# Performance work log

Measured on AMD Instinct MI355X. Metric: run time of the kernel, lower is better.

## Reference

```python
import jax, jax.numpy as jnp
import numpy as np

NT = 32          # nt_states
T = 64           # t_states
ST = NT + T      # total states
NEG = -1e9       # matches self.huge fill


def setup_inputs() -> dict:
    key = jax.random.key(0)
    k1, k2, k3 = jax.random.split(key, 3)
    B, n = 8, 28
    return {
        "unary_scores": jax.random.normal(k1, (B, n, T), dtype=jnp.float32),
        "rule_scores": jax.random.normal(k2, (B, NT, ST, ST), dtype=jnp.float32),
        "root_scores": jax.random.normal(k3, (B, NT), dtype=jnp.float32),
    }


def _inside(unary_scores, rule_scores, root_scores):
    # Chart indexed beta[b, width, start, state]; span (s, s+w) lives at [b, w, s].
    # Invalid (state-range) slots hold NEG, so exp() underflows them to exactly 0,
    # reproducing the terminal/nonterminal slice logic of the torch code.
    B, n, _ = unary_scores.shape
    beta = jnp.full((B, n, n, ST), NEG, dtype=unary_scores.dtype)
    beta = beta.at[:, 0, :, NT:].set(unary_scores)  # width-0 diagonal: preterminals

    mrule = rule_scores.max(axis=(2, 3))                    # [B, A]
    erule = jnp.exp(rule_scores - mrule[:, :, None, None])  # [B, A, L, R]

    for w in range(1, n):
        S = n - w                     # number of valid start positions
        k = np.arange(w)              # split offset: u = s + k
        # left child: span (s, s+k) -> width k, start s
        left = beta[:, :w, :S, :]                                  # [B, w, S, ST]
        # right child: span (s+k+1, s+w) -> width w-1-k, start s+k+1
        sr = k[:, None] + 1 + np.arange(S)[None, :]                # [w, S]
        right = beta[:, (w - 1 - k)[:, None], sr, :]               # [B, w, S, ST]

        # stable logsumexp over (k, l, r) via exp-space matmuls
        ml = left.max(-1)                                          # [B, w, S]
        mr = right.max(-1)                                         # [B, w, S]
        M = (ml + mr).max(1)                                       # [B, S]
        el = jnp.exp(left - ml[..., None])
        er = jnp.exp(right - mr[..., None] + (ml + mr - M[:, None, :])[..., None])
        numer = jnp.einsum('bksl,bksr->bslr', el, er)              # [B, S, L, R]
        total = jnp.einsum('bslr,balr->bsa', numer, erule)         # [B, S, A]
        score = jnp.log(total) + M[..., None] + mrule[:, None, :]
        beta = beta.at[:, w, :S, :NT].set(score)

    top = beta[:, n - 1, 0, :NT] + root_scores                     # span (0, n-1)
    return jax.nn.logsumexp(top, axis=1)                           # log Z, [B]


def reference(unary_scores, rule_scores, root_scores):
    return _inside(unary_scores, rule_scores, root_scores)
```

## Files before the change

### kernel.cpp

```cpp
#include <hip/hip_runtime.h>
#include <cstdint>
#include <cstddef>


#define NMAX 28
#define SLOTT 864
#define SLOTN 3456

#define R_ELT 0
#define R_F   1856
#define R_G   5568
#define R_F2  9280
#define R_G2  12992
#define R_TRI 16704
#define R_BMX 22736
#define R_ENA 23520
#define C_TRI 0
#define C_BMX 6032
#define C_GPP 6816
#define C_ELK 7584
#define C_ERK 8608
#define C_NUM 14752
#define C_RED 16536
#define LDSF  27616

__device__ __forceinline__ int off32(int w, int n) {
    return (w - 1) * n - (w * (w - 1)) / 2;
}
__device__ __forceinline__ float gload(const float* p) {
    return __hip_atomic_load(p, __ATOMIC_RELAXED, __HIP_MEMORY_SCOPE_AGENT);
}
__device__ __forceinline__ void gstore(float* p, float v) {
    __hip_atomic_store(p, v, __ATOMIC_RELAXED, __HIP_MEMORY_SCOPE_AGENT);
}
__device__ __forceinline__ unsigned gloadu(const unsigned* p) {
    return __hip_atomic_load(p, __ATOMIC_RELAXED, __HIP_MEMORY_SCOPE_AGENT);
}
__device__ __forceinline__ void gstoreu(unsigned* p, unsigned v) {
    __hip_atomic_store(p, v, __ATOMIC_RELAXED, __HIP_MEMORY_SCOPE_AGENT);
}
__device__ __forceinline__ float dot4acc(float4 m, float4 t, float acc) {
    return fmaf(m.x, t.x, fmaf(m.y, t.y, fmaf(m.z, t.z, fmaf(m.w, t.w, acc))));
}
__device__ __forceinline__ float b2f(unsigned short u) {
    return __uint_as_float(((unsigned)u) << 16);
}
__device__ __forceinline__ unsigned short f2b(float x) {
    unsigned u = __float_as_uint(x);
    return (unsigned short)((u + 0x7fffu + ((u >> 16) & 1u)) >> 16);
}
__device__ __forceinline__ float maxM(const float* bmx, int w, int s) {
    float M = -3.0e38f;
    for (int k = 0; k < w; ++k)
        M = fmaxf(M, bmx[k * NMAX + s] + bmx[(w - 1 - k) * NMAX + s + k + 1]);
    return M;
}
__device__ __forceinline__ float maxMc(const float* bmx, int w, int s) {
    float M = -3.0e38f;
    for (int k = 2; k <= w - 3; ++k)
        M = fmaxf(M, bmx[k * NMAX + s] + bmx[(w - 1 - k) * NMAX + s + k + 1]);
    return M;
}
__device__ __forceinline__ void finalize_row(float* lds, int triOff, int bmxOff,
                                             const float* slot, int wf, int n,
                                             int tid) {
    int Sp = n - wf;
    if (tid < Sp * 32) {
        int s = tid >> 5, aa = tid & 31;
        float q = gload(slot + s * 32 + aa);
        float m2 = q;
        for (int off = 16; off > 0; off >>= 1)
            m2 = fmaxf(m2, __shfl_xor(m2, off, 32));
        ((unsigned short*)(lds + triOff))[(off32(wf, n) + s) * 32 + aa] = f2b(q / m2);
        if (aa == 0)
            lds[bmxOff + wf * NMAX + s] = __logf(m2) + maxM(lds + bmxOff, wf, s);
    }
}

__global__ __launch_bounds__(256) void prep_kernel(const float* __restrict__ unary,
                                                   float* __restrict__ elT_g,
                                                   float* __restrict__ bmax0_g,
                                                   unsigned* __restrict__ flags,
                                                   int n) {
    int b = blockIdx.x, tid = threadIdx.x;
    if (tid < 16) gstoreu(&flags[b * 32 + tid], (tid >= 8) ? 4u : 0u);
    for (int pos = tid >> 6; pos < n; pos += 4) {
        int t = tid & 63;
        float v = unary[((size_t)(b * n) + pos) * 64 + t];
        float m = v;
        for (int off = 32; off > 0; off >>= 1) m = fmaxf(m, __shfl_xor(m, off, 64));
        elT_g[(size_t)b * 64 * n + t * n + pos] = __expf(v - m);
        if (t == 0) bmax0_g[b * 32 + pos] = m;
    }
}

__global__ __launch_bounds__(256) void pack_kernel(const float* __restrict__ rule,
                                                   const float* __restrict__ elT_g,
                                                   float* __restrict__ H_g,
                                                   float* __restrict__ F_g,
                                                   float* __restrict__ G_g,
                                                   float* __restrict__ ENa_g,
                                                   float* __restrict__ ENc_g,
                                                   int n) {
    extern __shared__ float sl[];
    int b = blockIdx.y, aa = blockIdx.x, tid = threadIdx.x;
    const int ag = aa >> 2, a4 = aa & 3;
    const float4* rs4 = (const float4*)(rule + (size_t)(b * 32 + aa) * 9216);
    for (int i = tid; i < 2304; i += 256) {
        float4 v = rs4[i];
        float4 o;
        o.x = __expf(v.x); o.y = __expf(v.y); o.z = __expf(v.z); o.w = __expf(v.w);
        ((float4*)sl)[i] = o;
    }
    for (int i = tid; i < 64 * n; i += 256)
        sl[9216 + i] = elT_g[(size_t)b * 64 * n + i];
    __syncthreads();
    const float* elt = sl + 9216;
    if (tid < 256) {
        int flat = tid * 4, l = flat >> 5, r = flat & 31;
        float4 o = *(const float4*)(sl + l * 96 + r);
        *(float4*)(ENc_g + ((size_t)(b * 256 + tid) * 32 + aa) * 4) = o;
    }
    for (int i = tid; i < 1024; i += 256)
        ENa_g[((size_t)(b * 8 + ag) * 4096) + a4 * 1024 + i] = sl[(i >> 5) * 96 + (i & 31)];
    for (int i = tid; i < 64 * n; i += 256) {
        int r = i / n, s = i - r * n;
        float acc = 0.f;
        for (int l = 0; l < 64; ++l)
            acc = fmaf(elt[l * n + s], sl[(32 + l) * 96 + 32 + r], acc);
        H_g[(size_t)(b * 8 + ag) * 7424 + (r * 29 + s) * 4 + a4] = acc;
    }
    for (int i = tid; i < 32 * n; i += 256) {
        int r = i / n, s = i - r * n;
        float acc = 0.f;
        for (int l = 0; l < 64; ++l)
            acc = fmaf(elt[l * n + s], sl[(32 + l) * 96 + r], acc);
        F_g[(size_t)(b * 8 + ag) * 3712 + (r * 29 + s) * 4 + a4] = acc;
    }
    for (int i = tid; i < 32 * n; i += 256) {
        int l = i / n, s = i - l * n;
        float acc = 0.f;
        for (int r = 0; r < 64; ++r)
            acc = fmaf(elt[r * n + s], sl[l * 96 + 32 + r], acc);
        G_g[(size_t)(b * 8 + ag) * 3712 + (l * 29 + s) * 4 + a4] = acc;
    }
}

__global__ __launch_bounds__(1024, 1) void inside_kernel(
    const float* __restrict__ elT_g, const float* __restrict__ bmax0_g,
    const float* __restrict__ H_g, const float* __restrict__ F_g,
    const float* __restrict__ G_g, const float* __restrict__ ENa_g,
    const float* __restrict__ ENc_g,
    float* __restrict__ ringT, float* __restrict__ ringN,
    const float* __restrict__ root, float* __restrict__ out,
    unsigned* __restrict__ flags, int n) {
    extern __shared__ float lds[];
    const int b = blockIdx.x >> 4, ch = blockIdx.x & 15;
    const int tid = threadIdx.x;
    unsigned* const fl = flags + b * 32;
    float* const rT = ringT + (size_t)b * 8 * SLOTT;
    float* const rN = ringN + (size_t)b * 4 * SLOTN;

    if (ch < 8) {
        for (int i = tid; i < 64 * n; i += 1024) {
            int t = i / n, pos = i - t * n;
            lds[R_ELT + t * 29 + pos] = elT_g[(size_t)b * 64 * n + i];
        }
        for (int i = tid; i < 3712; i += 1024) lds[R_F + i] = F_g[(size_t)(b * 8 + ch) * 3712 + i];
        for (int i = tid; i < 3712; i += 1024) lds[R_G + i] = G_g[(size_t)(b * 8 + ch) * 3712 + i];
        for (int i = tid; i < 7424; i += 1024) lds[R_F2 + i] = H_g[(size_t)(b * 8 + ch) * 7424 + i];
        for (int i = tid; i < 4096; i += 1024) lds[R_ENA + i] = ENa_g[(size_t)(b * 8 + ch) * 4096 + i];
        if (tid < n) lds[R_BMX + tid] = bmax0_g[b * 32 + tid];
        __syncthreads();

        for (int w = 1; w < n; ++w) {
            const int S = n - w;
            if (tid < 64) {
                unsigned tgt = 0u;
                if (tid < 8) tgt = (w >= 2) ? (unsigned)(w - 1) : 0u;
                else if (tid < 16 && w >= 5) {
                    int p = (tid - 8) >> 2;
                    if (p == (w & 1)) tgt = (unsigned)w;
                }
                for (;;) {
                    unsigned v = (tid < 16) ? gloadu(&fl[tid]) : 0u;
                    if (__ballot(v < tgt) == 0ull) break;
                    __builtin_amdgcn_s_sleep(1);
                }
            }
            __syncthreads();

            if (w >= 2)
                finalize_row(lds, R_TRI, R_BMX, rT + (size_t)((w - 1) & 7) * SLOTT,
                             w - 1, n, tid);
            __syncthreads();

            if (w == 2) {
                const unsigned short* tri = (const unsigned short*)(lds + R_TRI);
                const int b1 = off32(1, n);
                for (int i = tid; i < 32 * 29 * 4; i += 1024) {
                    int a4 = i & 3, rest = i >> 2, s = rest % 29, rl = rest / 29;
                    if (s < n - 1) {
                        float accF = 0.f, accG = 0.f;
                        for (int q = 0; q < 32; ++q) {
                            float e1 = b2f(tri[(b1 + s) * 32 + q]);
                            accF = fmaf(e1, lds[R_ENA + a4 * 1024 + q * 32 + rl], accF);
                            accG = fmaf(lds[R_ENA + a4 * 1024 + rl * 32 + q], e1, accG);
                        }
                        lds[R_F2 + (rl * 29 + s) * 4 + a4] = accF;
                        lds[R_G2 + (rl * 29 + s) * 4 + a4] = accG;
                    }
                }
                __syncthreads();
            }

            if (tid < S * 4) {
                int s = tid >> 2, a4 = tid & 3, a = ch * 4 + a4;
                float cr0 = 0.f, cr1 = 0.f, cr2 = 0.f, cr3 = 0.f;
                if (w >= 5) {
                    const float* p = rN + (size_t)(w & 3) * SLOTN + (size_t)(s * 32 + a) * 4;
                    cr0 = gload(p); cr1 = gload(p + 1); cr2 = gload(p + 2); cr3 = gload(p + 3);
                }
                float M = maxM(lds + R_BMX, w, s);
                const unsigned short* tri = (const unsigned short*)(lds + R_TRI);
                float t2;
                if (w == 1) {
                    float acc = 0.f;
                    for (int r = 0; r < 64; ++r)
                        acc = fmaf(lds[R_ELT + r * 29 + s + 1],
                                   lds[R_F2 + (r * 29 + s) * 4 + a4], acc);
                    t2 = acc;
                } else {
                    int b1 = off32(w - 1, n);
                    float aTN = 0.f, aNT = 0.f;
                    for (int r = 0; r < 32; ++r)
                        aTN = fmaf(b2f(tri[(b1 + s + 1) * 32 + r]),
                                   lds[R_F + (r * 29 + s) * 4 + a4], aTN);
                    for (int l = 0; l < 32; ++l)
                        aNT = fmaf(b2f(tri[(b1 + s) * 32 + l]),
                                   lds[R_G + (l * 29 + s + w) * 4 + a4], aNT);
                    float g0 = __expf(lds[R_BMX + s] + lds[R_BMX + (w - 1) * NMAX + s + 1] - M);
                    float gw = __expf(lds[R_BMX + (w - 1) * NMAX + s] + lds[R_BMX + s + w] - M);
                    t2 = aTN * g0 + aNT * gw;
                    if (w >= 3) {
                        int b2 = off32(w - 2, n);
                        float e1 = 0.f;
                        for (int r = 0; r < 32; ++r)
                            e1 = fmaf(b2f(tri[(b2 + s + 2) * 32 + r]),
                                      lds[R_F2 + (r * 29 + s) * 4 + a4], e1);
                        t2 = fmaf(e1, __expf(lds[R_BMX + NMAX + s] +
                                             lds[R_BMX + (w - 2) * NMAX + s + 2] - M), t2);
                        if (w >= 4) {
                            float e2 = 0.f;
                            for (int l = 0; l < 32; ++l)
                                e2 = fmaf(b2f(tri[(b2 + s) * 32 + l]),
                                          lds[R_G2 + (l * 29 + s + w - 1) * 4 + a4], e2);
                            t2 = fmaf(e2, __expf(lds[R_BMX + (w - 2) * NMAX + s] +
                                                 lds[R_BMX + NMAX + s + w - 1] - M), t2);
                        }
                    }
                    if (w >= 5) {
                        float Mc = maxMc(lds + R_BMX, w, s);
                        t2 = fmaf(((cr0 + cr1) + (cr2 + cr3)), __expf(Mc - M), t2);
                    }
                }
                gstore(rT + (size_t)(w & 7) * SLOTT + s * 32 + a, t2);
            }
            __syncthreads();
            if (tid == 0) gstoreu(&fl[ch], (unsigned)w);
        }

        if (ch == 0) {
            if (tid < 64) {
                unsigned tgt = (unsigned)(n - 1);
                for (;;) {
                    unsigned v = (tid < 8) ? gloadu(&fl[tid]) : tgt;
                    if (__ballot(v < tgt) == 0ull) break;
                    __builtin_amdgcn_s_sleep(1);
                }
            }
            __syncthreads();
            if (tid < 32) {
                float q = gload(rT + (size_t)((n - 1) & 7) * SLOTT + tid);
                float v = q * __expf(root[b * 32 + tid]);
                for (int off = 16; off > 0; off >>= 1) v += __shfl_xor(v, off, 32);
                if (tid == 0) out[b] = maxM(lds + R_BMX, n - 1, 0) + __logf(v);
            }
        }
    } else {
        const int idx = ch - 8, slice = idx & 3, par = idx >> 2;
        float4 e4;
        {
            int g = tid >> 5, a = tid & 31;
            e4 = *(const float4*)(ENc_g + ((size_t)(b * 256 + slice * 32 + g) * 32 + a) * 4);
        }
        if (tid < n) lds[C_BMX + tid] = bmax0_g[b * 32 + tid];
        __syncthreads();
        int lastFin = 0;
        const int W0 = (par == 1) ? 5 : 6;
        for (int W = W0; W < n; W += 2) {
            const int S = n - W, Sp2 = S | 1;
            const int cnt = W - 4;
            int q4 = (cnt + 3) >> 2; if (!(q4 & 1)) ++q4;
            const int K4 = 4 * q4;
            if (tid < 64) {
                unsigned tgt = (unsigned)(W - 3);
                for (;;) {
                    unsigned v = (tid < 8) ? gloadu(&fl[tid]) : tgt;
                    if (__ballot(v < tgt) == 0ull) break;
                    __builtin_amdgcn_s_sleep(1);
                }
            }
            __syncthreads();
            for (int wf = lastFin + 1; wf <= W - 3; ++wf) {
                finalize_row(lds, C_TRI, C_BMX, rT + (size_t)(wf & 7) * SLOTT, wf, n, tid);
                __syncthreads();
            }
            lastFin = W - 3;
            if (tid < cnt * 32) {
                int k = (tid >> 5) + 2, s = tid & 31;
                if (s < S) {
                    float Mc = maxMc(lds + C_BMX, W, s);
                    lds[C_GPP + (k - 2) * 32 + s] =
                        __expf(lds[C_BMX + k * NMAX + s] +
                               lds[C_BMX + (W - 1 - k) * NMAX + s + k + 1] - Mc);
                }
            }
            __syncthreads();
            if (tid < S * 32) {
                int s = tid >> 5, sym = tid & 31;
                const unsigned short* tri = (const unsigned short*)(lds + C_TRI);
                int eo = (sym * Sp2 + s) * K4;
                for (int k = 2; k <= W - 3; ++k)
                    lds[C_ERK + eo + k - 2] =
                        b2f(tri[(off32(W - 1 - k, n) + s + k + 1) * 32 + sym]) *
                        lds[C_GPP + (k - 2) * 32 + s];
                for (int j = cnt; j < K4; ++j) lds[C_ERK + eo + j] = 0.f;
                if (sym < 4) {
                    int lo = (sym * Sp2 + s) * K4;
                    int gl = slice * 4 + sym;
                    for (int k = 2; k <= W - 3; ++k)
                        lds[C_ELK + lo + k - 2] = b2f(tri[(off32(k, n) + s) * 32 + gl]);
                    for (int j = cnt; j < K4; ++j) lds[C_ELK + lo + j] = 0.f;
                }
            }
            __syncthreads();
            {
                int cL = tid & 127, sh = tid >> 7;
                int lloc = cL >> 5, r = cL & 31;
                unsigned short* np = (unsigned short*)(lds + C_NUM);
                for (int s = sh; s < S; s += 8) {
                    const float* ep = lds + C_ELK + (lloc * Sp2 + s) * K4;
                    const float* rp = lds + C_ERK + (r * Sp2 + s) * K4;
                    float acc = 0.f;
                    for (int j = 0; j < K4; j += 4)
                        acc = dot4acc(*(const float4*)(ep + j), *(const float4*)(rp + j), acc);
                    np[s * 132 + cL] = f2b(acc);
                }
            }
            __syncthreads();
            {
                const unsigned short* np = (const unsigned short*)(lds + C_NUM);
                unsigned short* red = (unsigned short*)(lds + C_RED);
                int g = tid >> 5, a = tid & 31, wv = tid >> 6;
                bool low = (tid & 32) == 0;
                for (int s = 0; s < S; ++s) {
                    const unsigned short* pp = np + s * 132 + g * 4;
                    float acc = b2f(pp[0]) * e4.x + b2f(pp[1]) * e4.y +
                                b2f(pp[2]) * e4.z + b2f(pp[3]) * e4.w;
                    acc += __shfl_xor(acc, 32, 64);
                    if (low) red[wv * 896 + s * 32 + a] = f2b(acc);
                }
            }
            __syncthreads();
            if (tid < S * 32) {
                const unsigned short* red = (const unsigned short*)(lds + C_RED);
                float t = 0.f;
                for (int g2 = 0; g2 < 16; ++g2) t += b2f(red[g2 * 896 + tid]);
                gstore(rN + (size_t)(W & 3) * SLOTN + (size_t)tid * 4 + slice, t);
            }
            __syncthreads();
            if (tid == 0) gstoreu(&fl[ch], (unsigned)W);
        }
    }
}

extern "C" void kernel_launch(void* const* d_in, const int* in_sizes, int n_in,
                              void* d_out, int out_size, void* d_ws, size_t ws_size,
                              hipStream_t stream) {
    const float* unary = (const float*)d_in[0];
    const float* rule  = (const float*)d_in[1];
    const float* root  = (const float*)d_in[2];
    float* out = (float*)d_out;

    const int B = in_sizes[2] / 32;
    int n = in_sizes[0] / (B * 64);

    float* ws = (float*)d_ws;
    float* elT_g = ws;
    float* bmax0 = elT_g + (size_t)B * 64 * n;
    float* H_g   = bmax0 + (size_t)B * 32;
    float* F_g   = H_g + (size_t)B * 8 * 7424;
    float* G_g   = F_g + (size_t)B * 8 * 3712;
    float* ENa_g = G_g + (size_t)B * 8 * 3712;
    float* ENc_g = ENa_g + (size_t)B * 8 * 4096;
    float* ringT = ENc_g + (size_t)B * 32768;
    float* ringN = ringT + (size_t)B * 8 * SLOTT;
    unsigned* flags = (unsigned*)(ringN + (size_t)B * 4 * SLOTN);

    prep_kernel<<<dim3(B), 256, 0, stream>>>(unary, elT_g, bmax0, flags, n);

    const int packLds = (9216 + 64 * n) * 4;
    hipFuncSetAttribute((const void*)pack_kernel,
                        hipFuncAttributeMaxDynamicSharedMemorySize, packLds);
    pack_kernel<<<dim3(32, B), 256, packLds, stream>>>(rule, elT_g, H_g, F_g,
                                                       G_g, ENa_g, ENc_g, n);

    hipFuncSetAttribute((const void*)inside_kernel,
                        hipFuncAttributeMaxDynamicSharedMemorySize, LDSF * 4);
    void* args[] = {
        (void*)&elT_g, (void*)&bmax0, (void*)&H_g, (void*)&F_g, (void*)&G_g,
        (void*)&ENa_g, (void*)&ENc_g, (void*)&ringT, (void*)&ringN,
        (void*)&root, (void*)&out, (void*)&flags, (void*)&n
    };
    hipLaunchCooperativeKernel((void*)inside_kernel, dim3(B * 16), dim3(1024),
                               args, LDSF * 4, stream);
}
```

Measured before the change: 260.8 us.

## Split inside-step dot products across 8 lanes, store fp32 tri, widen consumer slices

The producer blocks now spread each (start, state) dot product over 8 threads using float4 LDS reads and a shuffle reduction, where before one thread ran a serial 32- to 64-step loop. The triangular chart is kept in fp32 rather than bf16, so the LDS layout grows. Ring-buffer loads are issued early and batched before the finalize work. Consumer blocks handle 8 left states per slice instead of 4 and fold the gamma precompute pass into the ERK fill, removing a barrier. The cost is more LDS, a different assignment of work to consumer channels, and extra shuffle reductions.

```diff
diff --git a/kernel.cpp b/kernel.cpp
--- a/kernel.cpp
+++ b/kernel.cpp
@@ -13,16 +13,15 @@
 #define R_F2  9280
 #define R_G2  12992
 #define R_TRI 16704
-#define R_BMX 22736
-#define R_ENA 23520
+#define R_BMX 28768
+#define R_ENA 29552
 #define C_TRI 0
-#define C_BMX 6032
-#define C_GPP 6816
-#define C_ELK 7584
-#define C_ERK 8608
-#define C_NUM 14752
-#define C_RED 16536
-#define LDSF  27616
+#define C_BMX 12064
+#define C_ELK 12848
+#define C_ERK 14896
+#define C_NUM 22192
+#define C_RED 25704
+#define LDSF  33648
 
 __device__ __forceinline__ int off32(int w, int n) {
     return (w - 1) * n - (w * (w - 1)) / 2;
@@ -60,21 +59,6 @@
     for (int k = 2; k <= w - 3; ++k)
         M = fmaxf(M, bmx[k * NMAX + s] + bmx[(w - 1 - k) * NMAX + s + k + 1]);
     return M;
-}
-__device__ __forceinline__ void finalize_row(float* lds, int triOff, int bmxOff,
-                                             const float* slot, int wf, int n,
-                                             int tid) {
-    int Sp = n - wf;
-    if (tid < Sp * 32) {
-        int s = tid >> 5, aa = tid & 31;
-        float q = gload(slot + s * 32 + aa);
-        float m2 = q;
-        for (int off = 16; off > 0; off >>= 1)
-            m2 = fmaxf(m2, __shfl_xor(m2, off, 32));
-        ((unsigned short*)(lds + triOff))[(off32(wf, n) + s) * 32 + aa] = f2b(q / m2);
-        if (aa == 0)
-            lds[bmxOff + wf * NMAX + s] = __logf(m2) + maxM(lds + bmxOff, wf, s);
-    }
 }
 
 __global__ __launch_bounds__(256) void prep_kernel(const float* __restrict__ unary,
@@ -175,6 +159,8 @@
 
         for (int w = 1; w < n; ++w) {
             const int S = n - w;
+            const int q = tid >> 3, lane8 = tid & 7;
+
             if (tid < 64) {
                 unsigned tgt = 0u;
                 if (tid < 8) tgt = (w >= 2) ? (unsigned)(w - 1) : 0u;
@@ -190,22 +176,37 @@
             }
             __syncthreads();
 
-            if (w >= 2)
-                finalize_row(lds, R_TRI, R_BMX, rT + (size_t)((w - 1) & 7) * SLOTT,
-                             w - 1, n, tid);
+            float crPre = 0.f, qf = 0.f;
+            if (w >= 5 && lane8 < 4 && q < S * 4) {
+                int s0 = q >> 2, aa = ch * 4 + (q & 3);
+                crPre = gload(rN + (size_t)(w & 3) * SLOTN +
+                              (size_t)(s0 * 32 + aa) * 4 + lane8);
+            }
+            if (w >= 2 && tid < (S + 1) * 32)
+                qf = gload(rT + (size_t)((w - 1) & 7) * SLOTT + tid);
+
+            if (w >= 2 && tid < (S + 1) * 32) {
+                int s = tid >> 5, aa = tid & 31;
+                float m2 = qf;
+                for (int off = 16; off > 0; off >>= 1)
+                    m2 = fmaxf(m2, __shfl_xor(m2, off, 32));
+                lds[R_TRI + (off32(w - 1, n) + s) * 32 + aa] = qf / m2;
+                if (aa == 0)
+                    lds[R_BMX + (w - 1) * NMAX + s] =
+                        __logf(m2) + maxM(lds + R_BMX, w - 1, s);
+            }
             __syncthreads();
 
             if (w == 2) {
-                const unsigned short* tri = (const unsigned short*)(lds + R_TRI);
                 const int b1 = off32(1, n);
                 for (int i = tid; i < 32 * 29 * 4; i += 1024) {
                     int a4 = i & 3, rest = i >> 2, s = rest % 29, rl = rest / 29;
                     if (s < n - 1) {
                         float accF = 0.f, accG = 0.f;
-                        for (int q = 0; q < 32; ++q) {
-                            float e1 = b2f(tri[(b1 + s) * 32 + q]);
-                            accF = fmaf(e1, lds[R_ENA + a4 * 1024 + q * 32 + rl], accF);
-                            accG = fmaf(lds[R_ENA + a4 * 1024 + rl * 32 + q], e1, accG);
+                        for (int qq = 0; qq < 32; ++qq) {
+                            float e1 = lds[R_TRI + (b1 + s) * 32 + qq];
+                            accF = fmaf(e1, lds[R_ENA + a4 * 1024 + qq * 32 + rl], accF);
+                            accG = fmaf(lds[R_ENA + a4 * 1024 + rl * 32 + qq], e1, accG);
                         }
                         lds[R_F2 + (rl * 29 + s) * 4 + a4] = accF;
                         lds[R_G2 + (rl * 29 + s) * 4 + a4] = accG;
@@ -214,57 +215,69 @@
                 __syncthreads();
             }
 
-            if (tid < S * 4) {
-                int s = tid >> 2, a4 = tid & 3, a = ch * 4 + a4;
-                float cr0 = 0.f, cr1 = 0.f, cr2 = 0.f, cr3 = 0.f;
-                if (w >= 5) {
-                    const float* p = rN + (size_t)(w & 3) * SLOTN + (size_t)(s * 32 + a) * 4;
-                    cr0 = gload(p); cr1 = gload(p + 1); cr2 = gload(p + 2); cr3 = gload(p + 3);
-                }
+            if (q < S * 4) {
+                const int s = q >> 2, a4 = q & 3, a = ch * 4 + a4;
                 float M = maxM(lds + R_BMX, w, s);
-                const unsigned short* tri = (const unsigned short*)(lds + R_TRI);
                 float t2;
                 if (w == 1) {
                     float acc = 0.f;
-                    for (int r = 0; r < 64; ++r)
-                        acc = fmaf(lds[R_ELT + r * 29 + s + 1],
+                    #pragma unroll
+                    for (int j = 0; j < 8; ++j) {
+                        int r = lane8 * 8 + j;
+                        acc = fmaf(lds[R_ELT + r * 29 + (s + 1)],
                                    lds[R_F2 + (r * 29 + s) * 4 + a4], acc);
+                    }
                     t2 = acc;
                 } else {
-                    int b1 = off32(w - 1, n);
-                    float aTN = 0.f, aNT = 0.f;
-                    for (int r = 0; r < 32; ++r)
-                        aTN = fmaf(b2f(tri[(b1 + s + 1) * 32 + r]),
-                                   lds[R_F + (r * 29 + s) * 4 + a4], aTN);
-                    for (int l = 0; l < 32; ++l)
-                        aNT = fmaf(b2f(tri[(b1 + s) * 32 + l]),
-                                   lds[R_G + (l * 29 + s + w) * 4 + a4], aNT);
-                    float g0 = __expf(lds[R_BMX + s] + lds[R_BMX + (w - 1) * NMAX + s + 1] - M);
-                    float gw = __expf(lds[R_BMX + (w - 1) * NMAX + s] + lds[R_BMX + s + w] - M);
+                    const float* tri = lds + R_TRI;
+                    const int b1o = off32(w - 1, n);
+                    const int r0 = lane8 * 4;
+                    float4 tv = *(const float4*)&tri[(b1o + s + 1) * 32 + r0];
+                    float aTN = tv.x * lds[R_F + ((r0 + 0) * 29 + s) * 4 + a4]
+                              + tv.y * lds[R_F + ((r0 + 1) * 29 + s) * 4 + a4]
+                              + tv.z * lds[R_F + ((r0 + 2) * 29 + s) * 4 + a4]
+                              + tv.w * lds[R_F + ((r0 + 3) * 29 + s) * 4 + a4];
+                    float4 lv = *(const float4*)&tri[(b1o + s) * 32 + r0];
+                    float aNT = lv.x * lds[R_G + ((r0 + 0) * 29 + s + w) * 4 + a4]
+                              + lv.y * lds[R_G + ((r0 + 1) * 29 + s + w) * 4 + a4]
+                              + lv.z * lds[R_G + ((r0 + 2) * 29 + s + w) * 4 + a4]
+                              + lv.w * lds[R_G + ((r0 + 3) * 29 + s + w) * 4 + a4];
+                    float g0 = __expf(lds[R_BMX + s] +
+                                      lds[R_BMX + (w - 1) * NMAX + s + 1] - M);
+                    float gw = __expf(lds[R_BMX + (w - 1) * NMAX + s] +
+                                      lds[R_BMX + s + w] - M);
                     t2 = aTN * g0 + aNT * gw;
                     if (w >= 3) {
-                        int b2 = off32(w - 2, n);
-                        float e1 = 0.f;
-                        for (int r = 0; r < 32; ++r)
-                            e1 = fmaf(b2f(tri[(b2 + s + 2) * 32 + r]),
-                                      lds[R_F2 + (r * 29 + s) * 4 + a4], e1);
-                        t2 = fmaf(e1, __expf(lds[R_BMX + NMAX + s] +
-                                             lds[R_BMX + (w - 2) * NMAX + s + 2] - M), t2);
+                        const int b2o = off32(w - 2, n);
+                        float4 rv = *(const float4*)&tri[(b2o + s + 2) * 32 + r0];
+                        float e1 = rv.x * lds[R_F2 + ((r0 + 0) * 29 + s) * 4 + a4]
+                                 + rv.y * lds[R_F2 + ((r0 + 1) * 29 + s) * 4 + a4]
+                                 + rv.z * lds[R_F2 + ((r0 + 2) * 29 + s) * 4 + a4]
+                                 + rv.w * lds[R_F2 + ((r0 + 3) * 29 + s) * 4 + a4];
+                        float g1 = __expf(lds[R_BMX + NMAX + s] +
+                                          lds[R_BMX + (w - 2) * NMAX + s + 2] - M);
+                        t2 = fmaf(e1, g1, t2);
                         if (w >= 4) {
-                            float e2 = 0.f;
-                            for (int l = 0; l < 32; ++l)
-                                e2 = fmaf(b2f(tri[(b2 + s) * 32 + l]),
-                                          lds[R_G2 + (l * 29 + s + w - 1) * 4 + a4], e2);
-                            t2 = fmaf(e2, __expf(lds[R_BMX + (w - 2) * NMAX + s] +
-                                                 lds[R_BMX + NMAX + s + w - 1] - M), t2);
+                            float4 l2 = *(const float4*)&tri[(b2o + s) * 32 + r0];
+                            float e2 = l2.x * lds[R_G2 + ((r0 + 0) * 29 + s + w - 1) * 4 + a4]
+                                     + l2.y * lds[R_G2 + ((r0 + 1) * 29 + s + w - 1) * 4 + a4]
+                                     + l2.z * lds[R_G2 + ((r0 + 2) * 29 + s + w - 1) * 4 + a4]
+                                     + l2.w * lds[R_G2 + ((r0 + 3) * 29 + s + w - 1) * 4 + a4];
+                            float g2 = __expf(lds[R_BMX + (w - 2) * NMAX + s] +
+                                              lds[R_BMX + NMAX + s + w - 1] - M);
+                            t2 = fmaf(e2, g2, t2);
                         }
                     }
                     if (w >= 5) {
                         float Mc = maxMc(lds + R_BMX, w, s);
-                        t2 = fmaf(((cr0 + cr1) + (cr2 + cr3)), __expf(Mc - M), t2);
+                        t2 = fmaf(crPre, __expf(Mc - M), t2);
                     }
                 }
-                gstore(rT + (size_t)(w & 7) * SLOTT + s * 32 + a, t2);
+                t2 += __shfl_xor(t2, 1, 8);
+                t2 += __shfl_xor(t2, 2, 8);
+                t2 += __shfl_xor(t2, 4, 8);
+                if (lane8 == 0)
+                    gstore(rT + (size_t)(w & 7) * SLOTT + s * 32 + a, t2);
             }
             __syncthreads();
             if (tid == 0) gstoreu(&fl[ch], (unsigned)w);
@@ -281,18 +294,19 @@
             }
             __syncthreads();
             if (tid < 32) {
-                float q = gload(rT + (size_t)((n - 1) & 7) * SLOTT + tid);
-                float v = q * __expf(root[b * 32 + tid]);
+                float qv = gload(rT + (size_t)((n - 1) & 7) * SLOTT + tid);
+                float v = qv * __expf(root[b * 32 + tid]);
                 for (int off = 16; off > 0; off >>= 1) v += __shfl_xor(v, off, 32);
                 if (tid == 0) out[b] = maxM(lds + R_BMX, n - 1, 0) + __logf(v);
             }
         }
     } else {
         const int idx = ch - 8, slice = idx & 3, par = idx >> 2;
-        float4 e4;
+        float4 e4a, e4b;
         {
             int g = tid >> 5, a = tid & 31;
-            e4 = *(const float4*)(ENc_g + ((size_t)(b * 256 + slice * 32 + g) * 32 + a) * 4);
+            e4a = *(const float4*)(ENc_g + ((size_t)(b * 256 + slice * 64 + g * 2) * 32 + a) * 4);
+            e4b = *(const float4*)(ENc_g + ((size_t)(b * 256 + slice * 64 + g * 2 + 1) * 32 + a) * 4);
         }
         if (tid < n) lds[C_BMX + tid] = bmax0_g[b * 32 + tid];
         __syncthreads();
@@ -312,67 +326,92 @@
                 }
             }
             __syncthreads();
-            for (int wf = lastFin + 1; wf <= W - 3; ++wf) {
-                finalize_row(lds, C_TRI, C_BMX, rT + (size_t)(wf & 7) * SLOTT, wf, n, tid);
-                __syncthreads();
-            }
-            lastFin = W - 3;
-            if (tid < cnt * 32) {
-                int k = (tid >> 5) + 2, s = tid & 31;
-                if (s < S) {
-                    float Mc = maxMc(lds + C_BMX, W, s);
-                    lds[C_GPP + (k - 2) * 32 + s] =
-                        __expf(lds[C_BMX + k * NMAX + s] +
-                               lds[C_BMX + (W - 1 - k) * NMAX + s + k + 1] - Mc);
-                }
-            }
-            __syncthreads();
+
+            {
+                const int nf = (W - 3) - lastFin;
+                float qv[3];
+                for (int i = 0; i < nf; ++i) {
+                    int wf = lastFin + 1 + i;
+                    qv[i] = (tid < (n - wf) * 32)
+                        ? gload(rT + (size_t)(wf & 7) * SLOTT + tid) : 0.f;
+                }
+                for (int i = 0; i < nf; ++i) {
+                    int wf = lastFin + 1 + i;
+                    if (tid < (n - wf) * 32) {
+                        int s = tid >> 5, aa = tid & 31;
+                        float m2 = qv[i];
+                        for (int off = 16; off > 0; off >>= 1)
+                            m2 = fmaxf(m2, __shfl_xor(m2, off, 32));
+                        lds[C_TRI + (off32(wf, n) + s) * 32 + aa] = qv[i] / m2;
+                        if (aa == 0)
+                            lds[C_BMX + wf * NMAX + s] =
+                                __logf(m2) + maxM(lds + C_BMX, wf, s);
+                    }
+                    __syncthreads();
+                }
+                lastFin = W - 3;
+            }
+
             if (tid < S * 32) {
                 int s = tid >> 5, sym = tid & 31;
-                const unsigned short* tri = (const unsigned short*)(lds + C_TRI);
+                float Mc = maxMc(lds + C_BMX, W, s);
                 int eo = (sym * Sp2 + s) * K4;
                 for (int k = 2; k <= W - 3; ++k)
                     lds[C_ERK + eo + k - 2] =
-                        b2f(tri[(off32(W - 1 - k, n) + s + k + 1) * 32 + sym]) *
-                        lds[C_GPP + (k - 2) * 32 + s];
-                for (int j = cnt; j < K4; ++j) lds[C_ERK + eo + j] = 0.f;
-                if (sym < 4) {
+                        lds[C_TRI + (off32(W - 1 - k, n) + s + k + 1) * 32 + sym] *
+                        __expf(lds[C_BMX + k * NMAX + s] +
+                               lds[C_BMX + (W - 1 - k) * NMAX + s + k + 1] - Mc);
+                for (int j2 = cnt; j2 < K4; ++j2) lds[C_ERK + eo + j2] = 0.f;
+                if (sym < 8) {
                     int lo = (sym * Sp2 + s) * K4;
-                    int gl = slice * 4 + sym;
+                    int gl = slice * 8 + sym;
                     for (int k = 2; k <= W - 3; ++k)
-                        lds[C_ELK + lo + k - 2] = b2f(tri[(off32(k, n) + s) * 32 + gl]);
-                    for (int j = cnt; j < K4; ++j) lds[C_ELK + lo + j] = 0.f;
-                }
-            }
-            __syncthreads();
+                        lds[C_ELK + lo + k - 2] =
+                            lds[C_TRI + (off32(k, n) + s) * 32 + gl];
+                    for (int j2 = cnt; j2 < K4; ++j2) lds[C_ELK + lo + j2] = 0.f;
+                }
+            }
+            __syncthreads();
+
             {
-                int cL = tid & 127, sh = tid >> 7;
+                int cL = tid & 255, sh = tid >> 8;
                 int lloc = cL >> 5, r = cL & 31;
                 unsigned short* np = (unsigned short*)(lds + C_NUM);
-                for (int s = sh; s < S; s += 8) {
+                for (int s = sh; s < S; s += 4) {
                     const float* ep = lds + C_ELK + (lloc * Sp2 + s) * K4;
                     const float* rp = lds + C_ERK + (r * Sp2 + s) * K4;
                     float acc = 0.f;
                     for (int j = 0; j < K4; j += 4)
-                        acc = dot4acc(*(const float4*)(ep + j), *(const float4*)(rp + j), acc);
-                    np[s * 132 + cL] = f2b(acc);
-                }
-            }
-            __syncthreads();
+                        acc = dot4acc(*(const float4*)(ep + j),
+                                      *(const float4*)(rp + j), acc);
+                    np[s * 260 + cL] = f2b(acc);
+                }
+            }
+            __syncthreads();
+
             {
                 const unsigned short* np = (const unsigned short*)(lds + C_NUM);
                 unsigned short* red = (unsigned short*)(lds + C_RED);
                 int g = tid >> 5, a = tid & 31, wv = tid >> 6;
                 bool low = (tid & 32) == 0;
                 for (int s = 0; s < S; ++s) {
-                    const unsigned short* pp = np + s * 132 + g * 4;
-                    float acc = b2f(pp[0]) * e4.x + b2f(pp[1]) * e4.y +
-                                b2f(pp[2]) * e4.z + b2f(pp[3]) * e4.w;
+                    const unsigned short* pp = np + s * 260 + g * 8;
+                    uint2 u0 = *(const uint2*)pp;
+                    uint2 u1 = *(const uint2*)(pp + 4);
+                    #define LOu(x) __uint_as_float((x) << 16)
+                    #define HIu(x) __uint_as_float((x) & 0xffff0000u)
+                    float acc = LOu(u0.x) * e4a.x + HIu(u0.x) * e4a.y
+                              + LOu(u0.y) * e4a.z + HIu(u0.y) * e4a.w
+                              + LOu(u1.x) * e4b.x + HIu(u1.x) * e4b.y
+                              + LOu(u1.y) * e4b.z + HIu(u1.y) * e4b.w;
+                    #undef LOu
+                    #undef HIu
                     acc += __shfl_xor(acc, 32, 64);
                     if (low) red[wv * 896 + s * 32 + a] = f2b(acc);
                 }
             }
             __syncthreads();
+
             if (tid < S * 32) {
                 const unsigned short* red = (const unsigned short*)(lds + C_RED);
                 float t = 0.f;
```

Result: faster. 233.7 us (-10.4%).
